# Kernel optimization log

Hardware: AMD Instinct MI355X
Metric: run time of the kernel (lower is better)

## Reference

```python
import jax, jax.numpy as jnp
import numpy as np

B, S, D, E = 32, 16, 64, 768  # batch, max summary segments, max doc splits, embed dim
EPS = 1e-12


def _l2norm(x):
    # tf.nn.l2_normalize: x * rsqrt(max(sum(x^2), eps))
    return x * jax.lax.rsqrt(jnp.maximum(jnp.sum(x * x, axis=-1, keepdims=True), EPS))


def setup_inputs() -> dict:
    key = jax.random.key(0)
    ks = jax.random.split(key, 12)
    nd = jax.random.randint(ks[0], (B,), 1, D + 1)
    ns = jax.random.randint(ks[1], (B,), 1, S + 1)
    doc = jax.random.normal(ks[2], (B, D, E), jnp.float32)
    seg = jax.random.normal(ks[3], (B, S, E), jnp.float32)
    # emulate RaggedTensor.to_tensor(): zero padding beyond ragged lengths
    doc = doc * (jnp.arange(D)[None, :, None] < nd[:, None, None])
    seg = seg * (jnp.arange(S)[None, :, None] < ns[:, None, None])
    tis = jax.random.uniform(ks[4], (B, S), jnp.float32)
    tis = jnp.where(jnp.arange(S)[None, :] < ns[:, None], tis, 1.0)
    tagg = jax.random.uniform(ks[5], (B,), jnp.float32)
    s1, s2, s3 = 1.0 / np.sqrt(2 * E), 1.0 / np.sqrt(E), 1.0 / np.sqrt(E // 2)
    W1 = jax.random.normal(ks[6], (2 * E, E), jnp.float32) * s1
    W2 = jax.random.normal(ks[7], (E, E // 2), jnp.float32) * s2
    W3 = jax.random.normal(ks[8], (E // 2, 1), jnp.float32) * s3
    return {
        'document_splits_embedding': doc,
        'summary_sentences_embedding': seg,
        'num_document_splits': nd,
        'num_summary_segments': ns,
        'target_agg_score': tagg,
        'target_instance_score': tis,
        'W1': W1, 'b1': jnp.zeros((E,), jnp.float32),
        'W2': W2, 'b2': jnp.zeros((E // 2,), jnp.float32),
        'W3': W3, 'b3': jnp.zeros((1,), jnp.float32),
    }


def reference(document_splits_embedding, summary_sentences_embedding,
              num_document_splits, num_summary_segments,
              target_agg_score, target_instance_score,
              W1, b1, W2, b2, W3, b3):
    doc, seg = document_splits_embedding, summary_sentences_embedding
    nd, ns = num_document_splits, num_summary_segments
    b, d, e = doc.shape
    s = seg.shape[1]
    nsf = ns.astype(jnp.float32)

    # target_instance_score padded with 1.0 beyond ragged length (done in setup; pass through)
    tis = target_instance_score

    # ---- pairwise MLP over all (segment, doc_split) pairs ----
    pair = jnp.concatenate([
        jnp.broadcast_to(doc[:, None, :, :], (b, s, d, e)),
        jnp.broadcast_to(seg[:, :, None, :], (b, s, d, e)),
    ], axis=-1)                                             # [B,S,D,2E]
    h = jax.nn.gelu(pair @ W1 + b1, approximate=False)      # [B,S,D,E]
    h = jax.nn.gelu(h @ W2 + b2, approximate=False)         # [B,S,D,E/2]
    mlp_out = jax.nn.sigmoid(h @ W3 + b3)[..., 0]           # [B,S,D]

    doc_mask = (jnp.arange(d)[None, :] < nd[:, None]).astype(jnp.float32)  # [B,D]
    scored = doc_mask[:, None, :] * mlp_out                # mask invalid doc splits
    pred0 = jnp.max(scored, axis=2)                         # [B,S]
    seg_scale = jnp.where(ns > 10, 1.0, 100.0)[:, None]     # faithful to mask+(1-mask)*100
    pred = seg_scale * pred0                                # [B,S]

    # ---- cosine similarity prior (keras CosineSimilarity = -cos) ----
    dn = _l2norm(doc)                                       # [B,D,E]
    sn = _l2norm(seg)                                       # [B,S,E]
    cos = jnp.einsum('bse,bde->bsd', sn, dn)                # [B,S,D]
    sim = doc_mask[:, None, :] * (1.0 + (-cos)) / 2.0
    doc_cos = jnp.max(sim, axis=2)                          # [B,S]
    seg_mask = (jnp.arange(s)[None, :] < ns[:, None]).astype(jnp.float32)
    diff = jnp.abs(doc_cos - pred) * seg_mask
    cos_prior = jnp.mean(jnp.sum(diff, axis=1) / nsf)

    # ---- correlation prior: Pearson correlation over the 768 'sample' axis ----
    c = seg - jnp.mean(seg, axis=-1, keepdims=True)
    z = c * jax.lax.rsqrt(jnp.maximum(jnp.sum(c * c, axis=-1, keepdims=True), EPS))
    R = (1.0 + jnp.einsum('bse,bte->bst', z, z)) / 2.0      # [B,S,S]
    p = pred
    t1 = (1.0 - p)[:, :, None] * (1.0 - p)[:, None, :]
    t2 = p[:, :, None] * p[:, None, :]
    pair_mask = seg_mask[:, :, None] * seg_mask[:, None, :]
    term = jnp.abs(t1 - R) * jnp.abs(t2 - R) * pair_mask
    corr_prior = jnp.mean(jnp.sum(term, axis=(1, 2)) / nsf)

    return (target_agg_score, tis, pred, ns, cos_prior, corr_prior)
```

## Files before the change

kernel.cpp:

```cpp
#include <hip/hip_runtime.h>
#include <hip/hip_bf16.h>
#include <math.h>

#define EPSF 1e-12f

typedef short bf16x8 __attribute__((ext_vector_type(8)));
typedef float f32x4  __attribute__((ext_vector_type(4)));

__device__ __forceinline__ float gelu_fast(float x) {
    float x2 = x * x;
    float z = -2.3021184f * x * fmaf(0.044715f, x2, 1.0f);
    float u = __builtin_amdgcn_exp2f(z);
    return x * __builtin_amdgcn_rcpf(1.0f + u);
}
__device__ __forceinline__ float sigmoid_fast(float x) {
    float u = __builtin_amdgcn_exp2f(-1.44269504f * x);
    return __builtin_amdgcn_rcpf(1.0f + u);
}
__device__ __forceinline__ float bf2f(unsigned short u) {
    return __uint_as_float(((unsigned int)u) << 16);
}
__device__ __forceinline__ unsigned short f2bf(float f) {
    unsigned int u = __float_as_uint(f);
    u += 0x7FFFu + ((u >> 16) & 1u);
    return (unsigned short)(u >> 16);
}

__global__ __launch_bounds__(256) void k_prep(
    const float* __restrict__ doc, const float* __restrict__ seg,
    const float* __restrict__ W1, const float* __restrict__ W2,
    const float* __restrict__ tagg, const float* __restrict__ tis,
    const int* __restrict__ ns,
    float* __restrict__ dscale, float* __restrict__ sscale,
    float* __restrict__ smean, float* __restrict__ cscale,
    unsigned short* __restrict__ docB, unsigned short* __restrict__ segB,
    unsigned short* __restrict__ W1T, unsigned short* __restrict__ W2T,
    float* __restrict__ out)
{
    __shared__ float sT[64][65];
    int blk = blockIdx.x;
    int t = threadIdx.x;
    if (blk == 1000) {
        if (t < 32) out[t] = tagg[t];
        out[32 + t] = tis[t];
        out[32 + 256 + t] = tis[256 + t];
        if (t < 32) out[1056 + t] = (float)ns[t];
        return;
    }
    if (blk < 640) {
        int row = blk * 4 + (t >> 6);
        int lane = t & 63;
        const float* src = (row < 2048) ? (doc + (size_t)row * 768)
                                        : (seg + (size_t)(row - 2048) * 768);
        unsigned short* dst = (row < 2048) ? (docB + (size_t)row * 768)
                                           : (segB + (size_t)(row - 2048) * 768);
        float ss = 0.f, sm = 0.f;
        float4 v0 = *(const float4*)(src + lane * 4);
        float4 v1 = *(const float4*)(src + lane * 4 + 256);
        float4 v2 = *(const float4*)(src + lane * 4 + 512);
        ss += v0.x * v0.x + v0.y * v0.y + v0.z * v0.z + v0.w * v0.w;
        ss += v1.x * v1.x + v1.y * v1.y + v1.z * v1.z + v1.w * v1.w;
        ss += v2.x * v2.x + v2.y * v2.y + v2.z * v2.z + v2.w * v2.w;
        sm += v0.x + v0.y + v0.z + v0.w;
        sm += v1.x + v1.y + v1.z + v1.w;
        sm += v2.x + v2.y + v2.z + v2.w;
        {
            ushort4 o;
            o.x = f2bf(v0.x); o.y = f2bf(v0.y); o.z = f2bf(v0.z); o.w = f2bf(v0.w);
            *(ushort4*)(dst + lane * 4) = o;
            o.x = f2bf(v1.x); o.y = f2bf(v1.y); o.z = f2bf(v1.z); o.w = f2bf(v1.w);
            *(ushort4*)(dst + lane * 4 + 256) = o;
            o.x = f2bf(v2.x); o.y = f2bf(v2.y); o.z = f2bf(v2.z); o.w = f2bf(v2.w);
            *(ushort4*)(dst + lane * 4 + 512) = o;
        }
        #pragma unroll
        for (int off = 32; off > 0; off >>= 1) {
            ss += __shfl_down(ss, off);
            sm += __shfl_down(sm, off);
        }
        if (lane == 0) {
            if (row < 2048) {
                dscale[row] = rsqrtf(fmaxf(ss, EPSF));
            } else {
                int r = row - 2048;
                sscale[r] = rsqrtf(fmaxf(ss, EPSF));
                float mean = sm * (1.0f / 768.0f);
                smean[r] = mean;
                cscale[r] = rsqrtf(fmaxf(ss - sm * mean, EPSF));
            }
        }
        return;
    }
    int tt = blk - 640;
    const float* in; unsigned short* out2; int R, C, bx, by;
    if (tt < 288) { in = W1; out2 = W1T; R = 1536; C = 768; bx = tt % 12; by = tt / 12; }
    else { tt -= 288; in = W2; out2 = W2T; R = 768; C = 384; bx = tt % 6; by = tt / 6; }
    int c0 = bx * 64, r0 = by * 64;
    int tr = t >> 2, tc4 = (t & 3) * 16;
    #pragma unroll
    for (int i = 0; i < 4; ++i) {
        float4 v = *(const float4*)(in + (size_t)(r0 + tr) * C + c0 + tc4 + i * 4);
        sT[tr][tc4 + i * 4 + 0] = v.x; sT[tr][tc4 + i * 4 + 1] = v.y;
        sT[tr][tc4 + i * 4 + 2] = v.z; sT[tr][tc4 + i * 4 + 3] = v.w;
    }
    __syncthreads();
    union { uint4 v; unsigned short u[8]; } o0, o1;
    #pragma unroll
    for (int i = 0; i < 8; ++i) o0.u[i] = f2bf(sT[tc4 + i][tr]);
    #pragma unroll
    for (int i = 0; i < 8; ++i) o1.u[i] = f2bf(sT[tc4 + 8 + i][tr]);
    *(uint4*)(out2 + (size_t)(c0 + tr) * R + r0 + tc4) = o0.v;
    *(uint4*)(out2 + (size_t)(c0 + tr) * R + r0 + tc4 + 8) = o1.v;
}

__global__ __launch_bounds__(256) void k_l1(
    const unsigned short* __restrict__ docB, const unsigned short* __restrict__ segB,
    const unsigned short* __restrict__ W1T_bf, const float* __restrict__ b1,
    unsigned short* __restrict__ XdocB, unsigned short* __restrict__ XsegB)
{
    int mb = blockIdx.x;
    int n0 = blockIdx.y * 128;
    int t = threadIdx.x, w = t >> 6, l = t & 63;
    int lm = l & 15, kh = l >> 4;
    bool isdoc = (mb < 32);
    int m0 = isdoc ? mb * 64 : (mb - 32) * 64;
    const unsigned short* A = isdoc ? docB : segB;
    int koff = isdoc ? 0 : 768;
    unsigned short* C = isdoc ? XdocB : XsegB;

    const unsigned short* gA = A + (size_t)(m0 + lm) * 768 + kh * 8;
    const unsigned short* gB = W1T_bf + (size_t)(n0 + w * 32 + lm) * 1536 + koff + kh * 8;

    f32x4 acc[4][2];
    #pragma unroll
    for (int mt = 0; mt < 4; ++mt)
        #pragma unroll
        for (int nt = 0; nt < 2; ++nt) acc[mt][nt] = (f32x4){0.f, 0.f, 0.f, 0.f};

    bf16x8 a0A[4], a1A[4], b0A[2], b1A[2];
    bf16x8 a0B[4], a1B[4], b0B[2], b1B[2];
    #pragma unroll
    for (int mt = 0; mt < 4; ++mt) {
        a0A[mt] = *(const bf16x8*)(gA + (size_t)mt * 16 * 768);
        a1A[mt] = *(const bf16x8*)(gA + (size_t)mt * 16 * 768 + 32);
    }
    #pragma unroll
    for (int nt = 0; nt < 2; ++nt) {
        b0A[nt] = *(const bf16x8*)(gB + (size_t)nt * 16 * 1536);
        b1A[nt] = *(const bf16x8*)(gB + (size_t)nt * 16 * 1536 + 32);
    }

    #define L1_BODY(KT, A0, A1, B0, B1, NA0, NA1, NB0, NB1)                     \
    {                                                                           \
        if ((KT) < 11) {                                                        \
            int ko = ((KT) + 1) * 64;                                           \
            _Pragma("unroll")                                                   \
            for (int mt = 0; mt < 4; ++mt) {                                    \
                NA0[mt] = *(const bf16x8*)(gA + (size_t)mt * 16 * 768 + ko);    \
                NA1[mt] = *(const bf16x8*)(gA + (size_t)mt * 16 * 768 + ko + 32); \
            }                                                                   \
            _Pragma("unroll")                                                   \
            for (int nt = 0; nt < 2; ++nt) {                                    \
                NB0[nt] = *(const bf16x8*)(gB + (size_t)nt * 16 * 1536 + ko);   \
                NB1[nt] = *(const bf16x8*)(gB + (size_t)nt * 16 * 1536 + ko + 32); \
            }                                                                   \
        }                                                                       \
        _Pragma("unroll")                                                       \
        for (int mt = 0; mt < 4; ++mt)                                          \
            _Pragma("unroll")                                                   \
            for (int nt = 0; nt < 2; ++nt)                                      \
                acc[mt][nt] = __builtin_amdgcn_mfma_f32_16x16x32_bf16(          \
                    A0[mt], B0[nt], acc[mt][nt], 0, 0, 0);                      \
        _Pragma("unroll")                                                       \
        for (int mt = 0; mt < 4; ++mt)                                          \
            _Pragma("unroll")                                                   \
            for (int nt = 0; nt < 2; ++nt)                                      \
                acc[mt][nt] = __builtin_amdgcn_mfma_f32_16x16x32_bf16(          \
                    A1[mt], B1[nt], acc[mt][nt], 0, 0, 0);                      \
    }

    for (int kt2 = 0; kt2 < 12; kt2 += 2) {
        L1_BODY(kt2,     a0A, a1A, b0A, b1A, a0B, a1B, b0B, b1B);
        L1_BODY(kt2 + 1, a0B, a1B, b0B, b1B, a0A, a1A, b0A, b1A);
    }
    #undef L1_BODY

    #pragma unroll
    for (int nt = 0; nt < 2; ++nt) {
        int n = n0 + w * 32 + nt * 16 + lm;
        float bv = isdoc ? 0.f : b1[n];
        #pragma unroll
        for (int mt = 0; mt < 4; ++mt)
            #pragma unroll
            for (int j = 0; j < 4; ++j) {
                int row = m0 + mt * 16 + kh * 4 + j;
                C[(size_t)row * 768 + n] = f2bf(acc[mt][nt][j] + bv);
            }
    }
}

__global__ __launch_bounds__(256, 2) void k_fused_mfma(
    const unsigned short* __restrict__ XdocB, const unsigned short* __restrict__ XsegB,
    const unsigned short* __restrict__ W2T_bf,
    const float* __restrict__ b2, const float* __restrict__ W3, const float* __restrict__ b3,
    const int* __restrict__ nd, const int* __restrict__ ns,
    const unsigned short* __restrict__ docB, const unsigned short* __restrict__ segB,
    const float* __restrict__ seg,
    const float* __restrict__ dscale, const float* __restrict__ sscale,
    const float* __restrict__ smean, const float* __restrict__ cscale,
    float* __restrict__ out_pred, float* __restrict__ predv,
    float* __restrict__ dcws, float* __restrict__ Rws)
{
    __shared__ union {
        struct {
            unsigned short sA0[64 * 64];
            unsigned short sA1[64 * 64];
            float sXseg[768];
            float sRed[64][4];
        } p;
        struct { float sRedC[16][4]; } c;
        struct { unsigned short zb[16][776]; } r;
    } U;

    int blk = blockIdx.x;
    int t = threadIdx.x, w = t >> 6, l = t & 63;
    int lm = l & 15, kh = l >> 4;

    if (blk >= 512) {
        if (blk < 544) {
            int b = blk - 512;
            const unsigned short* gS = segB + (size_t)(b * 16 + lm) * 768 + kh * 8;
            const unsigned short* gD = docB + (size_t)(b * 64 + w * 16 + lm) * 768 + kh * 8;
            f32x4 acc = (f32x4){0.f, 0.f, 0.f, 0.f};
            for (int kt = 0; kt < 24; ++kt) {
                bf16x8 a = *(const bf16x8*)(gS + kt * 32);
                bf16x8 bb = *(const bf16x8*)(gD + kt * 32);
                acc = __builtin_amdgcn_mfma_f32_16x16x32_bf16(a, bb, acc, 0, 0, 0);
            }
            int ndb = nd[b];
            int d = w * 16 + lm;
            float dsc = dscale[b * 64 + d];
            #pragma unroll
            for (int j = 0; j < 4; ++j) {
                int s = kh * 4 + j;
                float cosv = acc[j] * sscale[b * 16 + s] * dsc;
                float sim = (d < ndb) ? (1.0f - cosv) * 0.5f : 0.f;
                sim = fmaxf(sim, __shfl_xor(sim, 1));
                sim = fmaxf(sim, __shfl_xor(sim, 2));
                sim = fmaxf(sim, __shfl_xor(sim, 4));
                sim = fmaxf(sim, __shfl_xor(sim, 8));
                if (lm == 0) U.c.sRedC[s][w] = sim;
            }
            __syncthreads();
            if (t < 16) {
                float dc = fmaxf(fmaxf(U.c.sRedC[t][0], U.c.sRedC[t][1]),
                                 fmaxf(U.c.sRedC[t][2], U.c.sRedC[t][3]));
                dcws[b * 16 + t] = dc;
            }
        } else {
            int b = blk - 544;
            for (int i = t; i < 16 * 768; i += 256) {
                int s = i / 768; int e = i - s * 768;
                U.r.zb[s][e] = f2bf((seg[((size_t)b * 16 + s) * 768 + e]
                                     - smean[b * 16 + s]) * cscale[b * 16 + s]);
            }
            __syncthreads();
            if (w == 0) {
                f32x4 acc = (f32x4){0.f, 0.f, 0.f, 0.f};
                #pragma unroll
                for (int kt = 0; kt < 24; ++kt) {
                    bf16x8 z = *(const bf16x8*)&U.r.zb[lm][kt * 32 + kh * 8];
                    acc = __builtin_amdgcn_mfma_f32_16x16x32_bf16(z, z, acc, 0, 0, 0);
                }
                #pragma unroll
                for (int j = 0; j < 4; ++j) {
                    int row = kh * 4 + j;
                    Rws[b * 256 + row * 16 + lm] = 0.5f * (1.0f + acc[j]);
                }
            }
        }
        return;
    }

    int bs = blk;
    int b = bs >> 4;
    int sw2 = (lm & 7) << 4;

    for (int i = t; i < 768; i += 256) U.p.sXseg[i] = bf2f(XsegB[(size_t)bs * 768 + i]);

    const int ndb = nd[b];
    const float segscale = (ns[b] > 10) ? 1.0f : 100.0f;
    const float b3v = b3[0];

    f32x4 acc[4][6];
    #pragma unroll
    for (int mt = 0; mt < 4; ++mt)
        #pragma unroll
        for (int nt = 0; nt < 6; ++nt) acc[mt][nt] = (f32x4){0.f, 0.f, 0.f, 0.f};

    int ar = t >> 2, ak = (t & 3) * 16;
    int asw = (ar & 7) << 4;
    const char* gXd = (const char*)XdocB + (size_t)(b * 64 + ar) * 1536;
    const unsigned short* gW2w = W2T_bf + (size_t)(w * 96 + lm) * 768 + kh * 8;

    union u128 { uint4 v; unsigned short u[8]; };

    bf16x8 bbA[6], bbB[6];
    #pragma unroll
    for (int nt = 0; nt < 6; ++nt)
        bbA[nt] = *(const bf16x8*)(gW2w + (size_t)nt * 16 * 768);

    {
        u128 xc0, xc1;
        xc0.v = *(const uint4*)(gXd + ak * 2);
        xc1.v = *(const uint4*)(gXd + ak * 2 + 16);
        __syncthreads();
        u128 o0, o1;
        #pragma unroll
        for (int i = 0; i < 8; ++i)
            o0.u[i] = f2bf(gelu_fast(bf2f(xc0.u[i]) + U.p.sXseg[ak + i]));
        #pragma unroll
        for (int i = 0; i < 8; ++i)
            o1.u[i] = f2bf(gelu_fast(bf2f(xc1.u[i]) + U.p.sXseg[ak + 8 + i]));
        *(uint4*)((char*)U.p.sA0 + ar * 128 + ((ak * 2) ^ asw)) = o0.v;
        *(uint4*)((char*)U.p.sA0 + ar * 128 + ((ak * 2 + 16) ^ asw)) = o1.v;
    }

    #pragma unroll
    for (int kt = 0; kt < 12; ++kt) {
        unsigned short* cbuf = (kt & 1) ? U.p.sA1 : U.p.sA0;
        unsigned short* nbuf = (kt & 1) ? U.p.sA0 : U.p.sA1;
        __syncthreads();
        u128 xn0, xn1;
        if (kt < 11) {
            xn0.v = *(const uint4*)(gXd + (kt + 1) * 128 + ak * 2);
            xn1.v = *(const uint4*)(gXd + (kt + 1) * 128 + ak * 2 + 16);
        }
        {
            #pragma unroll
            for (int nt = 0; nt < 6; ++nt)
                bbB[nt] = *(const bf16x8*)(gW2w + (size_t)nt * 16 * 768 + kt * 64 + 32);
            int kb = (kh * 16) ^ sw2;
            bf16x8 a[4];
            #pragma unroll
            for (int mt = 0; mt < 4; ++mt)
                a[mt] = *(const bf16x8*)((const char*)cbuf + (mt * 16 + lm) * 128 + kb);
            __builtin_amdgcn_s_setprio(1);
            #pragma unroll
            for (int mt = 0; mt < 4; ++mt)
                #pragma unroll
                for (int nt = 0; nt < 6; ++nt)
                    acc[mt][nt] = __builtin_amdgcn_mfma_f32_16x16x32_bf16(
                        a[mt], bbA[nt], acc[mt][nt], 0, 0, 0);
            __builtin_amdgcn_s_setprio(0);
        }
        {
            if (kt < 11) {
                #pragma unroll
                for (int nt = 0; nt < 6; ++nt)
                    bbA[nt] = *(const bf16x8*)(gW2w + (size_t)nt * 16 * 768 + (kt + 1) * 64);
            }
            int kb = (64 + kh * 16) ^ sw2;
            bf16x8 a[4];
            #pragma unroll
            for (int mt = 0; mt < 4; ++mt)
                a[mt] = *(const bf16x8*)((const char*)cbuf + (mt * 16 + lm) * 128 + kb);
            __builtin_amdgcn_s_setprio(1);
            #pragma unroll
            for (int mt = 0; mt < 4; ++mt)
                #pragma unroll
                for (int nt = 0; nt < 6; ++nt)
                    acc[mt][nt] = __builtin_amdgcn_mfma_f32_16x16x32_bf16(
                        a[mt], bbB[nt], acc[mt][nt], 0, 0, 0);
            __builtin_amdgcn_s_setprio(0);
        }
        if (kt < 11) {
            u128 o0, o1;
            #pragma unroll
            for (int i = 0; i < 8; ++i)
                o0.u[i] = f2bf(gelu_fast(bf2f(xn0.u[i]) + U.p.sXseg[(kt + 1) * 64 + ak + i]));
            #pragma unroll
            for (int i = 0; i < 8; ++i)
                o1.u[i] = f2bf(gelu_fast(bf2f(xn1.u[i]) + U.p.sXseg[(kt + 1) * 64 + ak + 8 + i]));
            *(uint4*)((char*)nbuf + ar * 128 + ((ak * 2) ^ asw)) = o0.v;
            *(uint4*)((char*)nbuf + ar * 128 + ((ak * 2 + 16) ^ asw)) = o1.v;
        }
    }

    float b2v[6], w3v[6];
    #pragma unroll
    for (int nt = 0; nt < 6; ++nt) {
        int n = w * 96 + nt * 16 + lm;
        b2v[nt] = b2[n]; w3v[nt] = W3[n];
    }
    #pragma unroll
    for (int mt = 0; mt < 4; ++mt) {
        #pragma unroll
        for (int j = 0; j < 4; ++j) {
            float s = 0.f;
            #pragma unroll
            for (int nt = 0; nt < 6; ++nt)
                s += gelu_fast(acc[mt][nt][j] + b2v[nt]) * w3v[nt];
            s += __shfl_xor(s, 1); s += __shfl_xor(s, 2);
            s += __shfl_xor(s, 4); s += __shfl_xor(s, 8);
            if (lm == 0) U.p.sRed[mt * 16 + kh * 4 + j][w] = s;
        }
    }
    __syncthreads();
    if (w == 0) {
        float h3 = U.p.sRed[l][0] + U.p.sRed[l][1] + U.p.sRed[l][2] + U.p.sRed[l][3] + b3v;
        float sig = sigmoid_fast(h3);
        float val = (l < ndb) ? sig : 0.f;
        #pragma unroll
        for (int off = 32; off > 0; off >>= 1) val = fmaxf(val, __shfl_xor(val, off));
        if (l == 0) {
            float pv = segscale * val;
            out_pred[bs] = pv;
            predv[bs] = pv;
        }
    }
}

__global__ __launch_bounds__(256) void k_final(
    const int* __restrict__ ns, const float* __restrict__ dcws,
    const float* __restrict__ Rws, const float* __restrict__ predv,
    float* __restrict__ out)
{
    __shared__ float sl1[32], sl2[32];
    int t = threadIdx.x;
    if (t < 32) {
        int nsb = ns[t];
        float sb = 0.f;
        #pragma unroll
        for (int s = 0; s < 16; ++s) {
            float d = fabsf(dcws[t * 16 + s] - predv[t * 16 + s]);
            sb += (s < nsb) ? d : 0.f;
        }
        sl1[t] = sb / (float)nsb;
    }
    {
        int b = t >> 3, c = t & 7;
        int nsb = ns[b];
        float sum = 0.f;
        #pragma unroll
        for (int k = 0; k < 32; ++k) {
            int idx = c * 32 + k;
            int s = idx >> 4, tt = idx & 15;
            float R = Rws[b * 256 + idx];
            float ps = predv[b * 16 + s], pt = predv[b * 16 + tt];
            float t1 = (1.f - ps) * (1.f - pt), t2 = ps * pt;
            float term = fabsf(t1 - R) * fabsf(t2 - R);
            sum += (s < nsb && tt < nsb) ? term : 0.f;
        }
        sum += __shfl_xor(sum, 1);
        sum += __shfl_xor(sum, 2);
        sum += __shfl_xor(sum, 4);
        if (c == 0) sl2[b] = sum / (float)nsb;
    }
    __syncthreads();
    if (t == 0) {
        float a = 0.f, bsum = 0.f;
        #pragma unroll
        for (int i = 0; i < 32; ++i) { a += sl1[i]; bsum += sl2[i]; }
        out[1088] = a * (1.0f / 32.0f);
        out[1089] = bsum * (1.0f / 32.0f);
    }
}

extern "C" void kernel_launch(void* const* d_in, const int* in_sizes, int n_in,
                              void* d_out, int out_size, void* d_ws, size_t ws_size,
                              hipStream_t stream)
{
    const float* doc  = (const float*)d_in[0];
    const float* seg  = (const float*)d_in[1];
    const int*   nd   = (const int*)d_in[2];
    const int*   ns   = (const int*)d_in[3];
    const float* tagg = (const float*)d_in[4];
    const float* tis  = (const float*)d_in[5];
    const float* W1   = (const float*)d_in[6];
    const float* b1   = (const float*)d_in[7];
    const float* W2   = (const float*)d_in[8];
    const float* b2   = (const float*)d_in[9];
    const float* W3   = (const float*)d_in[10];
    const float* b3   = (const float*)d_in[11];
    float* out = (float*)d_out;

    float* fws      = (float*)d_ws;
    float* dscale   = fws;
    float* sscale   = dscale + 2048;
    float* smean    = sscale + 512;
    float* cscale   = smean + 512;
    float* predv    = cscale + 512;
    float* dcws     = predv + 512;
    float* Rws      = dcws + 512;
    unsigned short* docB  = (unsigned short*)(Rws + 8192);
    unsigned short* segB  = docB + (size_t)2048 * 768;
    unsigned short* W1T   = segB + (size_t)512 * 768;
    unsigned short* W2T   = W1T + (size_t)768 * 1536;
    unsigned short* XdocB = W2T + (size_t)384 * 768;
    unsigned short* XsegB = XdocB + (size_t)2048 * 768;

    k_prep<<<1001, 256, 0, stream>>>(doc, seg, W1, W2, tagg, tis, ns,
                                     dscale, sscale, smean, cscale,
                                     docB, segB, W1T, W2T, out);
    k_l1<<<dim3(40, 6), 256, 0, stream>>>(docB, segB, W1T, b1, XdocB, XsegB);
    k_fused_mfma<<<576, 256, 0, stream>>>(XdocB, XsegB, W2T, b2, W3, b3, nd, ns,
                                          docB, segB, seg, dscale, sscale,
                                          smean, cscale, out + 544, predv,
                                          dcws, Rws);
    k_final<<<1, 256, 0, stream>>>(ns, dcws, Rws, predv, out);
}
```

Baseline: 82.58 us.

## Move cosine and correlation prior blocks from fused MLP kernel into prep kernel

The cosine-prior and correlation-matrix side blocks move out of the main MLP kernel and into the prep kernel as extra blocks. They now read fp32 inputs directly and compute the norms and means themselves, so the separate norm/mean workspace arrays are gone. This takes the 64 side blocks off the tail of the heavy MFMA kernel, letting it run only 512 uniform blocks, and lets that kernel use a simpler shared-memory layout. In exchange the prep kernel does more redundant fp32 reads and in-register bf16 conversion, and the norms are computed in separate passes.

```diff
diff --git a/kernel.cpp b/kernel.cpp
--- a/kernel.cpp
+++ b/kernel.cpp
@@ -30,23 +30,21 @@
     const float* __restrict__ doc, const float* __restrict__ seg,
     const float* __restrict__ W1, const float* __restrict__ W2,
     const float* __restrict__ tagg, const float* __restrict__ tis,
-    const int* __restrict__ ns,
-    float* __restrict__ dscale, float* __restrict__ sscale,
-    float* __restrict__ smean, float* __restrict__ cscale,
+    const int* __restrict__ ns, const int* __restrict__ nd,
     unsigned short* __restrict__ docB, unsigned short* __restrict__ segB,
     unsigned short* __restrict__ W1T, unsigned short* __restrict__ W2T,
-    float* __restrict__ out)
+    float* __restrict__ out, float* __restrict__ dcws, float* __restrict__ Rws)
 {
-    __shared__ float sT[64][65];
+    __shared__ union {
+        float sT[64][65];
+        struct { unsigned short zb[16][776]; float smL[16]; float csL[16]; } r;
+        struct { float sS16[16]; float sRedC[16][4]; } c;
+    } Up;
+
     int blk = blockIdx.x;
     int t = threadIdx.x;
-    if (blk == 1000) {
-        if (t < 32) out[t] = tagg[t];
-        out[32 + t] = tis[t];
-        out[32 + 256 + t] = tis[256 + t];
-        if (t < 32) out[1056 + t] = (float)ns[t];
-        return;
-    }
+    union u128 { uint4 v; unsigned short u[8]; };
+
     if (blk < 640) {
         int row = blk * 4 + (t >> 6);
         int lane = t & 63;
@@ -54,39 +52,117 @@
                                         : (seg + (size_t)(row - 2048) * 768);
         unsigned short* dst = (row < 2048) ? (docB + (size_t)row * 768)
                                            : (segB + (size_t)(row - 2048) * 768);
-        float ss = 0.f, sm = 0.f;
         float4 v0 = *(const float4*)(src + lane * 4);
         float4 v1 = *(const float4*)(src + lane * 4 + 256);
         float4 v2 = *(const float4*)(src + lane * 4 + 512);
-        ss += v0.x * v0.x + v0.y * v0.y + v0.z * v0.z + v0.w * v0.w;
-        ss += v1.x * v1.x + v1.y * v1.y + v1.z * v1.z + v1.w * v1.w;
-        ss += v2.x * v2.x + v2.y * v2.y + v2.z * v2.z + v2.w * v2.w;
-        sm += v0.x + v0.y + v0.z + v0.w;
-        sm += v1.x + v1.y + v1.z + v1.w;
-        sm += v2.x + v2.y + v2.z + v2.w;
-        {
-            ushort4 o;
-            o.x = f2bf(v0.x); o.y = f2bf(v0.y); o.z = f2bf(v0.z); o.w = f2bf(v0.w);
-            *(ushort4*)(dst + lane * 4) = o;
-            o.x = f2bf(v1.x); o.y = f2bf(v1.y); o.z = f2bf(v1.z); o.w = f2bf(v1.w);
-            *(ushort4*)(dst + lane * 4 + 256) = o;
-            o.x = f2bf(v2.x); o.y = f2bf(v2.y); o.z = f2bf(v2.z); o.w = f2bf(v2.w);
-            *(ushort4*)(dst + lane * 4 + 512) = o;
-        }
-        #pragma unroll
-        for (int off = 32; off > 0; off >>= 1) {
-            ss += __shfl_down(ss, off);
-            sm += __shfl_down(sm, off);
-        }
-        if (lane == 0) {
-            if (row < 2048) {
-                dscale[row] = rsqrtf(fmaxf(ss, EPSF));
-            } else {
-                int r = row - 2048;
-                sscale[r] = rsqrtf(fmaxf(ss, EPSF));
-                float mean = sm * (1.0f / 768.0f);
-                smean[r] = mean;
-                cscale[r] = rsqrtf(fmaxf(ss - sm * mean, EPSF));
+        ushort4 o;
+        o.x = f2bf(v0.x); o.y = f2bf(v0.y); o.z = f2bf(v0.z); o.w = f2bf(v0.w);
+        *(ushort4*)(dst + lane * 4) = o;
+        o.x = f2bf(v1.x); o.y = f2bf(v1.y); o.z = f2bf(v1.z); o.w = f2bf(v1.w);
+        *(ushort4*)(dst + lane * 4 + 256) = o;
+        o.x = f2bf(v2.x); o.y = f2bf(v2.y); o.z = f2bf(v2.z); o.w = f2bf(v2.w);
+        *(ushort4*)(dst + lane * 4 + 512) = o;
+        return;
+    }
+    if (blk == 1000) {
+        if (t < 32) out[t] = tagg[t];
+        out[32 + t] = tis[t];
+        out[32 + 256 + t] = tis[256 + t];
+        if (t < 32) out[1056 + t] = (float)ns[t];
+        return;
+    }
+    if (blk > 1000) {
+        int w = t >> 6, l = t & 63;
+        int lm = l & 15, kh = l >> 4;
+        if (blk < 1033) {
+            int b = blk - 1001;
+            const float* gS = seg + (size_t)(b * 16 + lm) * 768 + kh * 8;
+            const float* gD = doc + (size_t)(b * 64 + w * 16 + lm) * 768 + kh * 8;
+            f32x4 acc = (f32x4){0.f, 0.f, 0.f, 0.f};
+            float ssS = 0.f, ssD = 0.f;
+            for (int kt = 0; kt < 24; ++kt) {
+                float4 s0 = *(const float4*)(gS + kt * 32);
+                float4 s1 = *(const float4*)(gS + kt * 32 + 4);
+                float4 d0 = *(const float4*)(gD + kt * 32);
+                float4 d1 = *(const float4*)(gD + kt * 32 + 4);
+                ssS += s0.x*s0.x + s0.y*s0.y + s0.z*s0.z + s0.w*s0.w
+                     + s1.x*s1.x + s1.y*s1.y + s1.z*s1.z + s1.w*s1.w;
+                ssD += d0.x*d0.x + d0.y*d0.y + d0.z*d0.z + d0.w*d0.w
+                     + d1.x*d1.x + d1.y*d1.y + d1.z*d1.z + d1.w*d1.w;
+                u128 ua, ub;
+                ua.u[0] = f2bf(s0.x); ua.u[1] = f2bf(s0.y); ua.u[2] = f2bf(s0.z); ua.u[3] = f2bf(s0.w);
+                ua.u[4] = f2bf(s1.x); ua.u[5] = f2bf(s1.y); ua.u[6] = f2bf(s1.z); ua.u[7] = f2bf(s1.w);
+                ub.u[0] = f2bf(d0.x); ub.u[1] = f2bf(d0.y); ub.u[2] = f2bf(d0.z); ub.u[3] = f2bf(d0.w);
+                ub.u[4] = f2bf(d1.x); ub.u[5] = f2bf(d1.y); ub.u[6] = f2bf(d1.z); ub.u[7] = f2bf(d1.w);
+                acc = __builtin_amdgcn_mfma_f32_16x16x32_bf16(
+                    *(bf16x8*)&ua, *(bf16x8*)&ub, acc, 0, 0, 0);
+            }
+            ssS += __shfl_xor(ssS, 16); ssS += __shfl_xor(ssS, 32);
+            ssD += __shfl_xor(ssD, 16); ssD += __shfl_xor(ssD, 32);
+            float dscale_own = rsqrtf(fmaxf(ssD, EPSF));
+            if (w == 0 && kh == 0) Up.c.sS16[lm] = rsqrtf(fmaxf(ssS, EPSF));
+            __syncthreads();
+            int ndb = nd[b];
+            int d = w * 16 + lm;
+            #pragma unroll
+            for (int j = 0; j < 4; ++j) {
+                int s = kh * 4 + j;
+                float cosv = acc[j] * Up.c.sS16[s] * dscale_own;
+                float sim = (d < ndb) ? (1.0f - cosv) * 0.5f : 0.f;
+                sim = fmaxf(sim, __shfl_xor(sim, 1));
+                sim = fmaxf(sim, __shfl_xor(sim, 2));
+                sim = fmaxf(sim, __shfl_xor(sim, 4));
+                sim = fmaxf(sim, __shfl_xor(sim, 8));
+                if (lm == 0) Up.c.sRedC[s][w] = sim;
+            }
+            __syncthreads();
+            if (t < 16) {
+                float dc = fmaxf(fmaxf(Up.c.sRedC[t][0], Up.c.sRedC[t][1]),
+                                 fmaxf(Up.c.sRedC[t][2], Up.c.sRedC[t][3]));
+                dcws[b * 16 + t] = dc;
+            }
+        } else {
+            int b = blk - 1033;
+            #pragma unroll
+            for (int j = 0; j < 4; ++j) {
+                int r = w * 4 + j;
+                const float* src = seg + (size_t)(b * 16 + r) * 768;
+                float ss = 0.f, sm = 0.f;
+                #pragma unroll
+                for (int i = 0; i < 12; ++i) {
+                    float x = src[l + 64 * i];
+                    ss += x * x; sm += x;
+                }
+                #pragma unroll
+                for (int off = 32; off > 0; off >>= 1) {
+                    ss += __shfl_down(ss, off);
+                    sm += __shfl_down(sm, off);
+                }
+                if (l == 0) {
+                    float mean = sm * (1.0f / 768.0f);
+                    Up.r.smL[r] = mean;
+                    Up.r.csL[r] = rsqrtf(fmaxf(ss - sm * mean, EPSF));
+                }
+            }
+            __syncthreads();
+            for (int i = t; i < 16 * 768; i += 256) {
+                int s = i / 768; int e = i - s * 768;
+                Up.r.zb[s][e] = f2bf((seg[((size_t)b * 16 + s) * 768 + e]
+                                      - Up.r.smL[s]) * Up.r.csL[s]);
+            }
+            __syncthreads();
+            if (w == 0) {
+                f32x4 acc = (f32x4){0.f, 0.f, 0.f, 0.f};
+                #pragma unroll
+                for (int kt = 0; kt < 24; ++kt) {
+                    bf16x8 z = *(const bf16x8*)&Up.r.zb[lm][kt * 32 + kh * 8];
+                    acc = __builtin_amdgcn_mfma_f32_16x16x32_bf16(z, z, acc, 0, 0, 0);
+                }
+                #pragma unroll
+                for (int j = 0; j < 4; ++j) {
+                    int row = kh * 4 + j;
+                    Rws[b * 256 + row * 16 + lm] = 0.5f * (1.0f + acc[j]);
+                }
             }
         }
         return;
@@ -100,15 +176,15 @@
     #pragma unroll
     for (int i = 0; i < 4; ++i) {
         float4 v = *(const float4*)(in + (size_t)(r0 + tr) * C + c0 + tc4 + i * 4);
-        sT[tr][tc4 + i * 4 + 0] = v.x; sT[tr][tc4 + i * 4 + 1] = v.y;
-        sT[tr][tc4 + i * 4 + 2] = v.z; sT[tr][tc4 + i * 4 + 3] = v.w;
+        Up.sT[tr][tc4 + i * 4 + 0] = v.x; Up.sT[tr][tc4 + i * 4 + 1] = v.y;
+        Up.sT[tr][tc4 + i * 4 + 2] = v.z; Up.sT[tr][tc4 + i * 4 + 3] = v.w;
     }
     __syncthreads();
     union { uint4 v; unsigned short u[8]; } o0, o1;
     #pragma unroll
-    for (int i = 0; i < 8; ++i) o0.u[i] = f2bf(sT[tc4 + i][tr]);
-    #pragma unroll
-    for (int i = 0; i < 8; ++i) o1.u[i] = f2bf(sT[tc4 + 8 + i][tr]);
+    for (int i = 0; i < 8; ++i) o0.u[i] = f2bf(Up.sT[tc4 + i][tr]);
+    #pragma unroll
+    for (int i = 0; i < 8; ++i) o1.u[i] = f2bf(Up.sT[tc4 + 8 + i][tr]);
     *(uint4*)(out2 + (size_t)(c0 + tr) * R + r0 + tc4) = o0.v;
     *(uint4*)(out2 + (size_t)(c0 + tr) * R + r0 + tc4 + 8) = o1.v;
 }
@@ -204,89 +280,19 @@
     const unsigned short* __restrict__ W2T_bf,
     const float* __restrict__ b2, const float* __restrict__ W3, const float* __restrict__ b3,
     const int* __restrict__ nd, const int* __restrict__ ns,
-    const unsigned short* __restrict__ docB, const unsigned short* __restrict__ segB,
-    const float* __restrict__ seg,
-    const float* __restrict__ dscale, const float* __restrict__ sscale,
-    const float* __restrict__ smean, const float* __restrict__ cscale,
-    float* __restrict__ out_pred, float* __restrict__ predv,
-    float* __restrict__ dcws, float* __restrict__ Rws)
+    float* __restrict__ out_pred, float* __restrict__ predv)
 {
-    __shared__ union {
-        struct {
-            unsigned short sA0[64 * 64];
-            unsigned short sA1[64 * 64];
-            float sXseg[768];
-            float sRed[64][4];
-        } p;
-        struct { float sRedC[16][4]; } c;
-        struct { unsigned short zb[16][776]; } r;
-    } U;
-
-    int blk = blockIdx.x;
+    __shared__ unsigned short sA0[64 * 64];
+    __shared__ unsigned short sA1[64 * 64];
+    __shared__ float sXseg[768];
+    __shared__ float sRed[64][4];
+
+    int bs = blockIdx.x;
+    int b = bs >> 4;
     int t = threadIdx.x, w = t >> 6, l = t & 63;
-    int lm = l & 15, kh = l >> 4;
-
-    if (blk >= 512) {
-        if (blk < 544) {
-            int b = blk - 512;
-            const unsigned short* gS = segB + (size_t)(b * 16 + lm) * 768 + kh * 8;
-            const unsigned short* gD = docB + (size_t)(b * 64 + w * 16 + lm) * 768 + kh * 8;
-            f32x4 acc = (f32x4){0.f, 0.f, 0.f, 0.f};
-            for (int kt = 0; kt < 24; ++kt) {
-                bf16x8 a = *(const bf16x8*)(gS + kt * 32);
-                bf16x8 bb = *(const bf16x8*)(gD + kt * 32);
-                acc = __builtin_amdgcn_mfma_f32_16x16x32_bf16(a, bb, acc, 0, 0, 0);
-            }
-            int ndb = nd[b];
-            int d = w * 16 + lm;
-            float dsc = dscale[b * 64 + d];
-            #pragma unroll
-            for (int j = 0; j < 4; ++j) {
-                int s = kh * 4 + j;
-                float cosv = acc[j] * sscale[b * 16 + s] * dsc;
-                float sim = (d < ndb) ? (1.0f - cosv) * 0.5f : 0.f;
-                sim = fmaxf(sim, __shfl_xor(sim, 1));
-                sim = fmaxf(sim, __shfl_xor(sim, 2));
-                sim = fmaxf(sim, __shfl_xor(sim, 4));
-                sim = fmaxf(sim, __shfl_xor(sim, 8));
-                if (lm == 0) U.c.sRedC[s][w] = sim;
-            }
-            __syncthreads();
-            if (t < 16) {
-                float dc = fmaxf(fmaxf(U.c.sRedC[t][0], U.c.sRedC[t][1]),
-                                 fmaxf(U.c.sRedC[t][2], U.c.sRedC[t][3]));
-                dcws[b * 16 + t] = dc;
-            }
-        } else {
-            int b = blk - 544;
-            for (int i = t; i < 16 * 768; i += 256) {
-                int s = i / 768; int e = i - s * 768;
-                U.r.zb[s][e] = f2bf((seg[((size_t)b * 16 + s) * 768 + e]
-                                     - smean[b * 16 + s]) * cscale[b * 16 + s]);
-            }
-            __syncthreads();
-            if (w == 0) {
-                f32x4 acc = (f32x4){0.f, 0.f, 0.f, 0.f};
-                #pragma unroll
-                for (int kt = 0; kt < 24; ++kt) {
-                    bf16x8 z = *(const bf16x8*)&U.r.zb[lm][kt * 32 + kh * 8];
-                    acc = __builtin_amdgcn_mfma_f32_16x16x32_bf16(z, z, acc, 0, 0, 0);
-                }
-                #pragma unroll
-                for (int j = 0; j < 4; ++j) {
-                    int row = kh * 4 + j;
-                    Rws[b * 256 + row * 16 + lm] = 0.5f * (1.0f + acc[j]);
-                }
-            }
-        }
-        return;
-    }
-
-    int bs = blk;
-    int b = bs >> 4;
-    int sw2 = (lm & 7) << 4;
-
-    for (int i = t; i < 768; i += 256) U.p.sXseg[i] = bf2f(XsegB[(size_t)bs * 768 + i]);
+    int lm = l & 15, kh = l >> 4, sw2 = (lm & 7) << 4;
+
+    for (int i = t; i < 768; i += 256) sXseg[i] = bf2f(XsegB[(size_t)bs * 768 + i]);
 
     const int ndb = nd[b];
     const float segscale = (ns[b] > 10) ? 1.0f : 100.0f;
@@ -318,18 +324,18 @@
         u128 o0, o1;
         #pragma unroll
         for (int i = 0; i < 8; ++i)
-            o0.u[i] = f2bf(gelu_fast(bf2f(xc0.u[i]) + U.p.sXseg[ak + i]));
+            o0.u[i] = f2bf(gelu_fast(bf2f(xc0.u[i]) + sXseg[ak + i]));
         #pragma unroll
         for (int i = 0; i < 8; ++i)
-            o1.u[i] = f2bf(gelu_fast(bf2f(xc1.u[i]) + U.p.sXseg[ak + 8 + i]));
-        *(uint4*)((char*)U.p.sA0 + ar * 128 + ((ak * 2) ^ asw)) = o0.v;
-        *(uint4*)((char*)U.p.sA0 + ar * 128 + ((ak * 2 + 16) ^ asw)) = o1.v;
+            o1.u[i] = f2bf(gelu_fast(bf2f(xc1.u[i]) + sXseg[ak + 8 + i]));
+        *(uint4*)((char*)sA0 + ar * 128 + ((ak * 2) ^ asw)) = o0.v;
+        *(uint4*)((char*)sA0 + ar * 128 + ((ak * 2 + 16) ^ asw)) = o1.v;
     }
 
     #pragma unroll
     for (int kt = 0; kt < 12; ++kt) {
-        unsigned short* cbuf = (kt & 1) ? U.p.sA1 : U.p.sA0;
-        unsigned short* nbuf = (kt & 1) ? U.p.sA0 : U.p.sA1;
+        unsigned short* cbuf = (kt & 1) ? sA1 : sA0;
+        unsigned short* nbuf = (kt & 1) ? sA0 : sA1;
         __syncthreads();
         u128 xn0, xn1;
         if (kt < 11) {
@@ -378,10 +384,10 @@
             u128 o0, o1;
             #pragma unroll
             for (int i = 0; i < 8; ++i)
-                o0.u[i] = f2bf(gelu_fast(bf2f(xn0.u[i]) + U.p.sXseg[(kt + 1) * 64 + ak + i]));
+                o0.u[i] = f2bf(gelu_fast(bf2f(xn0.u[i]) + sXseg[(kt + 1) * 64 + ak + i]));
             #pragma unroll
             for (int i = 0; i < 8; ++i)
-                o1.u[i] = f2bf(gelu_fast(bf2f(xn1.u[i]) + U.p.sXseg[(kt + 1) * 64 + ak + 8 + i]));
+                o1.u[i] = f2bf(gelu_fast(bf2f(xn1.u[i]) + sXseg[(kt + 1) * 64 + ak + 8 + i]));
             *(uint4*)((char*)nbuf + ar * 128 + ((ak * 2) ^ asw)) = o0.v;
             *(uint4*)((char*)nbuf + ar * 128 + ((ak * 2 + 16) ^ asw)) = o1.v;
         }
@@ -403,12 +409,12 @@
                 s += gelu_fast(acc[mt][nt][j] + b2v[nt]) * w3v[nt];
             s += __shfl_xor(s, 1); s += __shfl_xor(s, 2);
             s += __shfl_xor(s, 4); s += __shfl_xor(s, 8);
-            if (lm == 0) U.p.sRed[mt * 16 + kh * 4 + j][w] = s;
+            if (lm == 0) sRed[mt * 16 + kh * 4 + j][w] = s;
         }
     }
     __syncthreads();
     if (w == 0) {
-        float h3 = U.p.sRed[l][0] + U.p.sRed[l][1] + U.p.sRed[l][2] + U.p.sRed[l][3] + b3v;
+        float h3 = sRed[l][0] + sRed[l][1] + sRed[l][2] + sRed[l][3] + b3v;
         float sig = sigmoid_fast(h3);
         float val = (l < ndb) ? sig : 0.f;
         #pragma unroll
@@ -485,14 +491,10 @@
     const float* b3   = (const float*)d_in[11];
     float* out = (float*)d_out;
 
-    float* fws      = (float*)d_ws;
-    float* dscale   = fws;
-    float* sscale   = dscale + 2048;
-    float* smean    = sscale + 512;
-    float* cscale   = smean + 512;
-    float* predv    = cscale + 512;
-    float* dcws     = predv + 512;
-    float* Rws      = dcws + 512;
+    float* fws   = (float*)d_ws;
+    float* predv = fws;
+    float* dcws  = predv + 512;
+    float* Rws   = dcws + 512;
     unsigned short* docB  = (unsigned short*)(Rws + 8192);
     unsigned short* segB  = docB + (size_t)2048 * 768;
     unsigned short* W1T   = segB + (size_t)512 * 768;
@@ -500,13 +502,10 @@
     unsigned short* XdocB = W2T + (size_t)384 * 768;
     unsigned short* XsegB = XdocB + (size_t)2048 * 768;
 
-    k_prep<<<1001, 256, 0, stream>>>(doc, seg, W1, W2, tagg, tis, ns,
-                                     dscale, sscale, smean, cscale,
-                                     docB, segB, W1T, W2T, out);
+    k_prep<<<1065, 256, 0, stream>>>(doc, seg, W1, W2, tagg, tis, ns, nd,
+                                     docB, segB, W1T, W2T, out, dcws, Rws);
     k_l1<<<dim3(40, 6), 256, 0, stream>>>(docB, segB, W1T, b1, XdocB, XsegB);
-    k_fused_mfma<<<576, 256, 0, stream>>>(XdocB, XsegB, W2T, b2, W3, b3, nd, ns,
-                                          docB, segB, seg, dscale, sscale,
-                                          smean, cscale, out + 544, predv,
-                                          dcws, Rws);
+    k_fused_mfma<<<512, 256, 0, stream>>>(XdocB, XsegB, W2T, b2, W3, b3, nd, ns,
+                                          out + 544, predv);
     k_final<<<1, 256, 0, stream>>>(ns, dcws, Rws, predv, out);
 }
```

Result: slower. 90.34 us (+9.4%).
